# Performance work log

Hardware: AMD Instinct MI355X
Metric: run time of the kernel (lower is better)

## Reference

```python
import jax, jax.numpy as jnp
import numpy as np

N_NODES = 50000
N_EDGES = 600000
IN_DIM = 128
OUT_DIM = 128
EPS = 1e-12  # guards sqrt grad at exactly-zero diffs (matches torch.norm subgradient behavior)


def setup_inputs() -> dict:
    key = jax.random.key(0)
    k1, k2, k3, k4, k5 = jax.random.split(key, 5)
    h = jax.random.normal(k1, (N_NODES, IN_DIM), dtype=jnp.float32)
    # xavier-uniform-ish scale for fc weight [out_dim, in_dim]
    lim = float(np.sqrt(6.0 / (IN_DIM + OUT_DIM)))
    W_fc = jax.random.uniform(k2, (OUT_DIM, IN_DIM), dtype=jnp.float32, minval=-lim, maxval=lim)
    beta = jax.random.uniform(k3, (1,), dtype=jnp.float32)  # Tensor(1).uniform_(0,1)
    src = jax.random.randint(k4, (N_EDGES,), 0, N_NODES, dtype=jnp.int32)
    dst = jax.random.randint(k5, (N_EDGES,), 0, N_NODES, dtype=jnp.int32)
    return {"h": h, "W_fc": W_fc, "beta": beta, "src": src, "dst": dst}


def reference(h, W_fc, beta, src, dst):
    n = h.shape[0]
    # z = fc(h)  (dropout omitted for determinism; see notes)
    z = h @ W_fc.T  # [N, out_dim]
    zs = z[src]     # [E, out_dim] gather
    zd = z[dst]     # [E, out_dim] gather
    # RBF edge attention: e = -beta * ||z_src - z_dst||_2
    sq = jnp.sum((zs - zd) ** 2, axis=1)          # [E]
    e = -beta[0] * jnp.sqrt(sq + EPS)             # [E]
    # segment softmax over incoming edges of each dst node
    m = jax.ops.segment_max(e, dst, num_segments=n)   # [N], -inf for empty
    ex = jnp.exp(e - m[dst])                          # [E]
    denom = jax.ops.segment_sum(ex, dst, num_segments=n)  # [N]
    alpha = ex / denom[dst]                           # [E]
    # scatter-weighted sum of src features into dst nodes
    h_out = jax.ops.segment_sum(alpha[:, None] * zs, dst, num_segments=n)  # [N, out_dim]
    return h_out
```

## Files before the change

### kernel.cpp

```cpp
#include <hip/hip_runtime.h>
#include <math.h>

#define N_NODES 50000
#define N_EDGES 600000
#define DIM 128
#define BCAP 64

typedef __attribute__((ext_vector_type(8))) short bf16x8;
typedef __attribute__((ext_vector_type(4))) float f32x4;

static __device__ __forceinline__ unsigned cvt_pk_bf16(float a, float b) {
    unsigned r;
    asm("v_cvt_pk_bf16_f32 %0, %1, %2" : "=v"(r) : "v"(a), "v"(b));
    return r;
}
static __device__ __forceinline__ unsigned short f2bf(float f) {
    return (unsigned short)cvt_pk_bf16(f, f);
}

#define UNPK(w, d0, d1)                         \
    d0 = __uint_as_float((w) << 16);            \
    d1 = __uint_as_float((w) & 0xFFFF0000u);

#define DPPADD(x, ctrl)                                                          \
    x += __int_as_float(__builtin_amdgcn_mov_dpp(__float_as_int(x), ctrl,        \
                                                 0xF, 0xF, true));
static __device__ __forceinline__ float row_sum16(float x) {
    DPPADD(x, 0xB1)
    DPPADD(x, 0x4E)
    DPPADD(x, 0x141)
    DPPADD(x, 0x140)
    return x;
}

__global__ __launch_bounds__(256) void prep_kernel(const float* __restrict__ W,
                                                   unsigned short* __restrict__ Wb,
                                                   int* __restrict__ cur,
                                                   int* __restrict__ cnt) {
    int gid = blockIdx.x * 256 + threadIdx.x;
    if (gid < N_NODES) {
        cur[gid] = 0;
        cnt[gid] = 0;
    }
    if (gid < DIM * DIM) Wb[gid] = f2bf(W[gid]);
}

static __device__ __forceinline__ void gemm_body(const float* __restrict__ h,
                                                 const unsigned short* __restrict__ Wb,
                                                 unsigned short* __restrict__ zb) {
    int wave = blockIdx.x * 4 + (threadIdx.x >> 6);
    if (wave >= N_NODES / 16) return;
    int lane = threadIdx.x & 63;
    int lo = lane & 15;
    int hi = lane >> 4;
    long row0 = (long)wave * 16;

    bf16x8 afrag[4];
    const float* arow = h + (row0 + lo) * DIM;
    #pragma unroll
    for (int kt = 0; kt < 4; ++kt) {
        const float* ap = arow + kt * 32 + hi * 8;
        float4 f0 = *(const float4*)ap;
        float4 f1 = *(const float4*)(ap + 4);
        union { unsigned u[4]; bf16x8 v; } c;
        c.u[0] = cvt_pk_bf16(f0.x, f0.y);
        c.u[1] = cvt_pk_bf16(f0.z, f0.w);
        c.u[2] = cvt_pk_bf16(f1.x, f1.y);
        c.u[3] = cvt_pk_bf16(f1.z, f1.w);
        afrag[kt] = c.v;
    }

    #pragma unroll
    for (int ct = 0; ct < 8; ++ct) {
        f32x4 acc = {0.f, 0.f, 0.f, 0.f};
        const unsigned short* brow = Wb + (ct * 16 + lo) * DIM + hi * 8;
        #pragma unroll
        for (int kt = 0; kt < 4; ++kt) {
            bf16x8 b = *(const bf16x8*)(brow + kt * 32);
            acc = __builtin_amdgcn_mfma_f32_16x16x32_bf16(afrag[kt], b, acc, 0, 0, 0);
        }
        unsigned short* zp = zb + (row0 + hi * 4) * DIM + ct * 16 + lo;
        zp[0 * DIM] = f2bf(acc[0]);
        zp[1 * DIM] = f2bf(acc[1]);
        zp[2 * DIM] = f2bf(acc[2]);
        zp[3 * DIM] = f2bf(acc[3]);
    }
}

__global__ __launch_bounds__(256) void gemm_fill_kernel(const float* __restrict__ h,
                                                        const unsigned short* __restrict__ Wb,
                                                        unsigned short* __restrict__ zb,
                                                        const int* __restrict__ src,
                                                        const int* __restrict__ dst,
                                                        int* __restrict__ cur,
                                                        int* __restrict__ lst) {
    int gid = blockIdx.x * 256 + threadIdx.x;
    int nth = gridDim.x * 256;
    for (int i = gid; i < N_EDGES; i += nth) {
        int d = dst[i];
        int pos = atomicAdd(cur + d, 1);
        if (pos < BCAP) lst[d * BCAP + pos] = src[i];
    }
    gemm_body(h, Wb, zb);
}

__global__ __launch_bounds__(256) void gemm_kernel(const float* __restrict__ h,
                                                   const unsigned short* __restrict__ Wb,
                                                   unsigned short* __restrict__ zb) {
    gemm_body(h, Wb, zb);
}

__global__ __launch_bounds__(256) void count_kernel(const int* __restrict__ dst,
                                                    int* __restrict__ cnt) {
    int i = blockIdx.x * 256 + threadIdx.x;
    if (i < N_EDGES) atomicAdd(cnt + dst[i], 1);
}

__global__ __launch_bounds__(256) void scan_a(const int* __restrict__ cnt,
                                              int* __restrict__ incl,
                                              int* __restrict__ bsum) {
    __shared__ int s[256];
    int i = blockIdx.x * 256 + threadIdx.x;
    s[threadIdx.x] = (i < N_NODES) ? cnt[i] : 0;
    __syncthreads();
    #pragma unroll
    for (int off = 1; off < 256; off <<= 1) {
        int t = (threadIdx.x >= off) ? s[threadIdx.x - off] : 0;
        __syncthreads();
        s[threadIdx.x] += t;
        __syncthreads();
    }
    if (i < N_NODES) incl[i] = s[threadIdx.x];
    if (threadIdx.x == 255) bsum[blockIdx.x] = s[255];
}

__global__ __launch_bounds__(256) void scan_b(int* __restrict__ bsum, int nb) {
    __shared__ int s[256];
    s[threadIdx.x] = (threadIdx.x < nb) ? bsum[threadIdx.x] : 0;
    __syncthreads();
    #pragma unroll
    for (int off = 1; off < 256; off <<= 1) {
        int t = (threadIdx.x >= off) ? s[threadIdx.x - off] : 0;
        __syncthreads();
        s[threadIdx.x] += t;
        __syncthreads();
    }
    if (threadIdx.x < nb) bsum[threadIdx.x] = s[threadIdx.x];
}

__global__ __launch_bounds__(256) void scan_c(int* __restrict__ incl_off,
                                              const int* __restrict__ cnt,
                                              const int* __restrict__ bsum) {
    int i = blockIdx.x * 256 + threadIdx.x;
    if (i >= N_NODES) return;
    int base = (blockIdx.x > 0) ? bsum[blockIdx.x - 1] : 0;
    incl_off[i] = incl_off[i] - cnt[i] + base;
}

__global__ __launch_bounds__(256) void cfill_kernel(const int* __restrict__ src,
                                                    const int* __restrict__ dst,
                                                    const int* __restrict__ off,
                                                    int* __restrict__ cur,
                                                    int* __restrict__ lst) {
    int i = blockIdx.x * 256 + threadIdx.x;
    if (i >= N_EDGES) return;
    int d = dst[i];
    int pos = atomicAdd(cur + d, 1);
    lst[off[d] + pos] = src[i];
}

__global__ __launch_bounds__(256) void node_kernel(const unsigned short* __restrict__ zb,
                                                   const int* __restrict__ lst,
                                                   const int* __restrict__ off,
                                                   const int* __restrict__ degp,
                                                   int stride,
                                                   const float* __restrict__ beta,
                                                   float* __restrict__ out) {
    int node = blockIdx.x * 4 + (threadIdx.x >> 6);
    if (node >= N_NODES) return;
    int lane = threadIdx.x & 63;
    int q = lane >> 4;
    int ql = lane & 15;
    int deg = degp[node];
    int start;
    if (stride > 0) {
        if (deg > BCAP) deg = BCAP;
        start = node * stride;
    } else {
        start = off[node];
    }
    float nbet = -beta[0];

    uint4 zdw = *(const uint4*)(zb + (long)node * DIM + ql * 8);
    float zd[8];
    UNPK(zdw.x, zd[0], zd[1]) UNPK(zdw.y, zd[2], zd[3])
    UNPK(zdw.z, zd[4], zd[5]) UNPK(zdw.w, zd[6], zd[7])

    float sden = 0.0f;
    float acc[8];
    #pragma unroll
    for (int i = 0; i < 8; ++i) acc[i] = 0.0f;

    for (int cb = 0; cb < deg; cb += 64) {
        int nch = deg - cb;
        if (nch > 64) nch = 64;
        int sj = (lane < nch) ? lst[start + cb + lane] : 0;

        for (int jb = 0; jb < nch; jb += 16) {
            int sv[4];
            bool vv[4];
            #pragma unroll
            for (int k = 0; k < 4; ++k) {
                int jo = jb + k * 4 + q;
                sv[k] = __shfl(sj, jo, 64);
                vv[k] = jo < nch;
            }
            uint4 aw[4];
            #pragma unroll
            for (int k = 0; k < 4; ++k)
                aw[k] = *(const uint4*)(zb + (long)sv[k] * DIM + ql * 8);

            #pragma unroll
            for (int k = 0; k < 4; ++k) {
                float a[8];
                UNPK(aw[k].x, a[0], a[1]) UNPK(aw[k].y, a[2], a[3])
                UNPK(aw[k].z, a[4], a[5]) UNPK(aw[k].w, a[6], a[7])
                float p = 0.0f;
                #pragma unroll
                for (int i = 0; i < 8; ++i) {
                    float d = a[i] - zd[i];
                    p += d * d;
                }
                p = row_sum16(p);
                float w = vv[k]
                        ? __expf(nbet * __builtin_amdgcn_sqrtf(p + 1e-12f))
                        : 0.0f;
                sden += w;
                #pragma unroll
                for (int i = 0; i < 8; ++i) acc[i] += w * a[i];
            }
        }
    }

    #define CMB(v) v += __shfl_xor(v, 16, 64); v += __shfl_xor(v, 32, 64);
    CMB(sden)
    CMB(acc[0]) CMB(acc[1]) CMB(acc[2]) CMB(acc[3])
    CMB(acc[4]) CMB(acc[5]) CMB(acc[6]) CMB(acc[7])
    #undef CMB

    float inv = (deg > 0) ? 1.0f / sden : 0.0f;
    if (q == 0) {
        float* orow = out + (long)node * DIM + ql * 8;
        *(float4*)orow =
            make_float4(acc[0] * inv, acc[1] * inv, acc[2] * inv, acc[3] * inv);
        *(float4*)(orow + 4) =
            make_float4(acc[4] * inv, acc[5] * inv, acc[6] * inv, acc[7] * inv);
    }
}

extern "C" void kernel_launch(void* const* d_in, const int* in_sizes, int n_in,
                              void* d_out, int out_size, void* d_ws, size_t ws_size,
                              hipStream_t stream) {
    const float* h    = (const float*)d_in[0];
    const float* W    = (const float*)d_in[1];
    const float* beta = (const float*)d_in[2];
    const int* src    = (const int*)d_in[3];
    const int* dst    = (const int*)d_in[4];
    float* out = (float*)d_out;

    const size_t bucket_total = (3200000ull + 3200000 + 150000 + 256 + 8192) * 4;
    const bool use_bucket = ws_size >= bucket_total;
    const size_t lst_len = use_bucket ? 3200000 : 600000;

    float* ws  = (float*)d_ws;
    unsigned short* zb = (unsigned short*)ws;
    int* lst   = (int*)(ws + 3200000);
    int* cnt   = (int*)(ws + 3200000 + lst_len);
    int* cur   = cnt + 50000;
    int* off   = cur + 50000;
    int* bsum  = off + 50000;
    unsigned short* Wb = (unsigned short*)(bsum + 256);

    const int gemm_blocks = (N_NODES / 16 + 3) / 4;

    prep_kernel<<<196, 256, 0, stream>>>(W, Wb, cur, cnt);
    if (use_bucket) {
        gemm_fill_kernel<<<gemm_blocks, 256, 0, stream>>>(h, Wb, zb, src, dst, cur, lst);
        node_kernel<<<N_NODES / 4, 256, 0, stream>>>(zb, lst, cur , cur, BCAP,
                                                     beta, out);
    } else {
        count_kernel<<<(N_EDGES + 255) / 256, 256, 0, stream>>>(dst, cnt);
        scan_a<<<196, 256, 0, stream>>>(cnt, off, bsum);
        scan_b<<<1, 256, 0, stream>>>(bsum, 196);
        scan_c<<<196, 256, 0, stream>>>(off, cnt, bsum);
        cfill_kernel<<<(N_EDGES + 255) / 256, 256, 0, stream>>>(src, dst, off, cur, lst);
        gemm_kernel<<<gemm_blocks, 256, 0, stream>>>(h, Wb, zb);
        node_kernel<<<N_NODES / 4, 256, 0, stream>>>(zb, lst, off, cnt, 0, beta, out);
    }
}
```

Measured before the change: 166.2 us.

## Map one node per quarter-wave and interleave fill/GEMM blocks

The node kernel now gives each 16-lane quarter of a wave its own destination node instead of splitting one node's edges across four quarters, which removes the cross-quarter shuffle reduction and the masked store. The fused fill+GEMM kernel is reshaped so that one in four blocks does GEMM rows while the other three each handle 256 edges of the bucket fill, instead of every block striding over edges and then running GEMM. The aim is better load balance and fewer idle lanes. The cost is divergence between the four nodes in a wave when their degrees differ, since the wave loops to the largest degree.

Result: slower. 173.2 us (+4.2%).

```diff
diff --git a/kernel.cpp b/kernel.cpp
--- a/kernel.cpp
+++ b/kernel.cpp
@@ -47,10 +47,8 @@
 
 static __device__ __forceinline__ void gemm_body(const float* __restrict__ h,
                                                  const unsigned short* __restrict__ Wb,
-                                                 unsigned short* __restrict__ zb) {
-    int wave = blockIdx.x * 4 + (threadIdx.x >> 6);
-    if (wave >= N_NODES / 16) return;
-    int lane = threadIdx.x & 63;
+                                                 unsigned short* __restrict__ zb,
+                                                 int wave, int lane) {
     int lo = lane & 15;
     int hi = lane >> 4;
     long row0 = (long)wave * 16;
@@ -87,27 +85,35 @@
     }
 }
 
-__global__ __launch_bounds__(256) void gemm_fill_kernel(const float* __restrict__ h,
-                                                        const unsigned short* __restrict__ Wb,
-                                                        unsigned short* __restrict__ zb,
-                                                        const int* __restrict__ src,
-                                                        const int* __restrict__ dst,
-                                                        int* __restrict__ cur,
-                                                        int* __restrict__ lst) {
-    int gid = blockIdx.x * 256 + threadIdx.x;
-    int nth = gridDim.x * 256;
-    for (int i = gid; i < N_EDGES; i += nth) {
-        int d = dst[i];
-        int pos = atomicAdd(cur + d, 1);
-        if (pos < BCAP) lst[d * BCAP + pos] = src[i];
-    }
-    gemm_body(h, Wb, zb);
+__global__ __launch_bounds__(256) void fg_kernel(const float* __restrict__ h,
+                                                 const unsigned short* __restrict__ Wb,
+                                                 unsigned short* __restrict__ zb,
+                                                 const int* __restrict__ src,
+                                                 const int* __restrict__ dst,
+                                                 int* __restrict__ cur,
+                                                 int* __restrict__ lst) {
+    int bid = blockIdx.x;
+    if (bid & 3) {
+        int f = (bid >> 2) * 3 + (bid & 3) - 1;
+        int i = f * 256 + threadIdx.x;
+        if (i < N_EDGES) {
+            int d = dst[i];
+            int pos = atomicAdd(cur + d, 1);
+            if (pos < BCAP) lst[d * BCAP + pos] = src[i];
+        }
+        return;
+    }
+    int wave = (bid >> 2) * 4 + (threadIdx.x >> 6);
+    if (wave >= N_NODES / 16) return;
+    gemm_body(h, Wb, zb, wave, threadIdx.x & 63);
 }
 
 __global__ __launch_bounds__(256) void gemm_kernel(const float* __restrict__ h,
                                                    const unsigned short* __restrict__ Wb,
                                                    unsigned short* __restrict__ zb) {
-    gemm_body(h, Wb, zb);
+    int wave = blockIdx.x * 4 + (threadIdx.x >> 6);
+    if (wave >= N_NODES / 16) return;
+    gemm_body(h, Wb, zb, wave, threadIdx.x & 63);
 }
 
 __global__ __launch_bounds__(256) void count_kernel(const int* __restrict__ dst,
@@ -176,11 +182,12 @@
                                                    int stride,
                                                    const float* __restrict__ beta,
                                                    float* __restrict__ out) {
-    int node = blockIdx.x * 4 + (threadIdx.x >> 6);
+    int wid  = blockIdx.x * 4 + (threadIdx.x >> 6);
+    int lane = threadIdx.x & 63;
+    int q    = lane >> 4;
+    int ql   = lane & 15;
+    int node = wid * 4 + q;
     if (node >= N_NODES) return;
-    int lane = threadIdx.x & 63;
-    int q = lane >> 4;
-    int ql = lane & 15;
     int deg = degp[node];
     int start;
     if (stride > 0) {
@@ -201,19 +208,19 @@
     #pragma unroll
     for (int i = 0; i < 8; ++i) acc[i] = 0.0f;
 
-    for (int cb = 0; cb < deg; cb += 64) {
+    for (int cb = 0; cb < deg; cb += 16) {
         int nch = deg - cb;
-        if (nch > 64) nch = 64;
-        int sj = (lane < nch) ? lst[start + cb + lane] : 0;
-
-        for (int jb = 0; jb < nch; jb += 16) {
+        if (nch > 16) nch = 16;
+        int sj = (ql < nch) ? lst[start + cb + ql] : 0;
+
+        for (int jb = 0; jb < nch; jb += 4) {
             int sv[4];
             bool vv[4];
             #pragma unroll
             for (int k = 0; k < 4; ++k) {
-                int jo = jb + k * 4 + q;
-                sv[k] = __shfl(sj, jo, 64);
+                int jo = jb + k;
                 vv[k] = jo < nch;
+                sv[k] = __shfl(sj, q * 16 + (vv[k] ? jo : 0), 64);
             }
             uint4 aw[4];
             #pragma unroll
@@ -242,20 +249,12 @@
         }
     }
 
-    #define CMB(v) v += __shfl_xor(v, 16, 64); v += __shfl_xor(v, 32, 64);
-    CMB(sden)
-    CMB(acc[0]) CMB(acc[1]) CMB(acc[2]) CMB(acc[3])
-    CMB(acc[4]) CMB(acc[5]) CMB(acc[6]) CMB(acc[7])
-    #undef CMB
-
     float inv = (deg > 0) ? 1.0f / sden : 0.0f;
-    if (q == 0) {
-        float* orow = out + (long)node * DIM + ql * 8;
-        *(float4*)orow =
-            make_float4(acc[0] * inv, acc[1] * inv, acc[2] * inv, acc[3] * inv);
-        *(float4*)(orow + 4) =
-            make_float4(acc[4] * inv, acc[5] * inv, acc[6] * inv, acc[7] * inv);
-    }
+    float* orow = out + (long)node * DIM + ql * 8;
+    *(float4*)orow =
+        make_float4(acc[0] * inv, acc[1] * inv, acc[2] * inv, acc[3] * inv);
+    *(float4*)(orow + 4) =
+        make_float4(acc[4] * inv, acc[5] * inv, acc[6] * inv, acc[7] * inv);
 }
 
 extern "C" void kernel_launch(void* const* d_in, const int* in_sizes, int n_in,
@@ -281,12 +280,12 @@
     int* bsum  = off + 50000;
     unsigned short* Wb = (unsigned short*)(bsum + 256);
 
-    const int gemm_blocks = (N_NODES / 16 + 3) / 4;
+    const int node_blocks = N_NODES / 16;
 
     prep_kernel<<<196, 256, 0, stream>>>(W, Wb, cur, cnt);
     if (use_bucket) {
-        gemm_fill_kernel<<<gemm_blocks, 256, 0, stream>>>(h, Wb, zb, src, dst, cur, lst);
-        node_kernel<<<N_NODES / 4, 256, 0, stream>>>(zb, lst, cur , cur, BCAP,
+        fg_kernel<<<3126, 256, 0, stream>>>(h, Wb, zb, src, dst, cur, lst);
+        node_kernel<<<node_blocks, 256, 0, stream>>>(zb, lst, cur , cur, BCAP,
                                                      beta, out);
     } else {
         count_kernel<<<(N_EDGES + 255) / 256, 256, 0, stream>>>(dst, cnt);
@@ -294,7 +293,7 @@
         scan_b<<<1, 256, 0, stream>>>(bsum, 196);
         scan_c<<<196, 256, 0, stream>>>(off, cnt, bsum);
         cfill_kernel<<<(N_EDGES + 255) / 256, 256, 0, stream>>>(src, dst, off, cur, lst);
-        gemm_kernel<<<gemm_blocks, 256, 0, stream>>>(h, Wb, zb);
-        node_kernel<<<N_NODES / 4, 256, 0, stream>>>(zb, lst, off, cnt, 0, beta, out);
-    }
-}
+        gemm_kernel<<<(N_NODES / 16 + 3) / 4, 256, 0, stream>>>(h, Wb, zb);
+        node_kernel<<<node_blocks, 256, 0, stream>>>(zb, lst, off, cnt, 0, beta, out);
+    }
+}
```
